# Performance work log

Measured on AMD Instinct MI355X. Metric: run time of the kernel, lower is better.

Reference implementation:

```python
import jax, jax.numpy as jnp
import numpy as np

N, E = 50000, 150000
IN, HID, LAT, EF, HE = 16, 32, 16, 8, 128


def _p(k, shape, fan_in):
    return jax.random.normal(k, shape, jnp.float32) / np.float32(np.sqrt(fan_in))


def setup_inputs() -> dict:
    key = jax.random.key(0)
    ks = jax.random.split(key, 32)
    inp = {
        "x": jax.random.normal(ks[0], (N, IN), jnp.float32),
        "edge_index": jax.random.randint(ks[1], (2, E), 0, N, dtype=jnp.int64),
        "edge_attr": jax.random.uniform(ks[2], (E, EF), jnp.float32),
    }
    # per-conv params: edge-MLP (w1,b1,w2,b2), root weight, bias
    dims = {"c1": (IN, HID), "c2": (HID, HID), "cmu": (HID, LAT), "clv": (HID, LAT)}
    i = 3
    for name, (din, dout) in dims.items():
        inp[f"{name}_w1"] = _p(ks[i], (EF, HE), EF)
        inp[f"{name}_b1"] = jnp.zeros((HE,), jnp.float32)
        inp[f"{name}_w2"] = _p(ks[i + 1], (HE, din * dout), HE)
        inp[f"{name}_b2"] = jnp.zeros((din * dout,), jnp.float32)
        inp[f"{name}_root"] = _p(ks[i + 2], (din, dout), din)
        inp[f"{name}_bias"] = jnp.zeros((dout,), jnp.float32)
        i += 3
    return inp


def _nnconv(x, src, dst, ea, w1, b1, w2, b2, root, bias, din, dout, mean):
    # edge MLP -> per-edge weight matrix [E, din, dout]
    h = jax.nn.relu(ea @ w1 + b1)
    W = (h @ w2 + b2).reshape(-1, din, dout)
    # gather source features, per-edge matmul, scatter-reduce to targets
    msg = jnp.einsum('ei,eio->eo', x[src], W)  # [E, dout]
    agg = jax.ops.segment_sum(msg, dst, num_segments=x.shape[0])
    if mean:
        cnt = jax.ops.segment_sum(jnp.ones((dst.shape[0],), x.dtype), dst,
                                  num_segments=x.shape[0])
        agg = agg / jnp.maximum(cnt, 1.0)[:, None]
    return agg + x @ root + bias


def reference(x, edge_index, edge_attr,
              c1_w1, c1_b1, c1_w2, c1_b2, c1_root, c1_bias,
              c2_w1, c2_b1, c2_w2, c2_b2, c2_root, c2_bias,
              cmu_w1, cmu_b1, cmu_w2, cmu_b2, cmu_root, cmu_bias,
              clv_w1, clv_b1, clv_w2, clv_b2, clv_root, clv_bias):
    src, dst = edge_index[0], edge_index[1]
    h = jax.nn.relu(_nnconv(x, src, dst, edge_attr, c1_w1, c1_b1, c1_w2, c1_b2,
                            c1_root, c1_bias, IN, HID, True))
    h = jax.nn.relu(_nnconv(h, src, dst, edge_attr, c2_w1, c2_b1, c2_w2, c2_b2,
                            c2_root, c2_bias, HID, HID, True))
    mu = _nnconv(h, src, dst, edge_attr, cmu_w1, cmu_b1, cmu_w2, cmu_b2,
                 cmu_root, cmu_bias, HID, LAT, False)
    logvar = _nnconv(h, src, dst, edge_attr, clv_w1, clv_b1, clv_w2, clv_b2,
                     clv_root, clv_bias, HID, LAT, False)
    return mu, logvar
```

## Files before the change

kernel.cpp:

```cpp
#include <hip/hip_runtime.h>

typedef __attribute__((ext_vector_type(8))) _Float16 half8;
typedef __attribute__((ext_vector_type(2))) _Float16 half2v;
typedef __attribute__((ext_vector_type(4))) float f32x4;

constexpr int NN  = 50000;
constexpr int NE  = 150000;
constexpr int IN  = 16;
constexpr int HID = 32;
constexpr int LAT = 16;
constexpr int EF  = 8;
constexpr int HE  = 128;
constexpr int NTILE = NE / 16;
constexpr int HSTR  = HE + 2;

constexpr int SCB = 256;
constexpr int NSB = (NN + SCB - 1) / SCB;

__global__ void count_kernel(const int* __restrict__ dst, int* __restrict__ cnt) {
  int e = blockIdx.x * blockDim.x + threadIdx.x;
  if (e < NE) atomicAdd(&cnt[dst[e]], 1);
}

__launch_bounds__(SCB)
__global__ void scan1(const int* __restrict__ cnt, int* __restrict__ bsum) {
  __shared__ int sdata[SCB];
  const int i = blockIdx.x * SCB + threadIdx.x;
  sdata[threadIdx.x] = (i < NN) ? cnt[i] : 0;
  __syncthreads();
  for (int off = SCB / 2; off > 0; off >>= 1) {
    if (threadIdx.x < off) sdata[threadIdx.x] += sdata[threadIdx.x + off];
    __syncthreads();
  }
  if (threadIdx.x == 0) bsum[blockIdx.x] = sdata[0];
}

__launch_bounds__(SCB)
__global__ void scan2(int* __restrict__ bsum) {
  __shared__ int sdata[SCB];
  const int t = threadIdx.x;
  const int v = (t < NSB) ? bsum[t] : 0;
  sdata[t] = v;
  __syncthreads();
  for (int off = 1; off < SCB; off <<= 1) {
    int u = (t >= off) ? sdata[t - off] : 0;
    __syncthreads();
    sdata[t] += u;
    __syncthreads();
  }
  if (t < NSB) bsum[t] = sdata[t] - v;
}

__launch_bounds__(SCB)
__global__ void scan3(const int* __restrict__ cnt, const int* __restrict__ bsum,
                      int* __restrict__ rowptr, int* __restrict__ wptr) {
  __shared__ int sdata[SCB];
  const int i = blockIdx.x * SCB + threadIdx.x;
  const int t = threadIdx.x;
  const int v = (i < NN) ? cnt[i] : 0;
  sdata[t] = v;
  __syncthreads();
  for (int off = 1; off < SCB; off <<= 1) {
    int u = (t >= off) ? sdata[t - off] : 0;
    __syncthreads();
    sdata[t] += u;
    __syncthreads();
  }
  const int excl = sdata[t] - v + bsum[blockIdx.x];
  if (i < NN) {
    rowptr[i] = excl;
    wptr[i]   = excl;
  }
  if (i == NN - 1) rowptr[NN] = NE;
}

__global__ void fill_kernel(const int* __restrict__ dst, int* __restrict__ wptr,
                            int* __restrict__ epos) {
  int e = blockIdx.x * blockDim.x + threadIdx.x;
  if (e < NE) epos[e] = atomicAdd(&wptr[dst[e]], 1);
}

__global__ void swizzle_kernel(const float* __restrict__ w2, const float* __restrict__ b2,
                               _Float16* __restrict__ w2h, int DIN_, int DOUT_) {
  int idx = blockIdx.x * blockDim.x + threadIdx.x;
  int tot = HSTR * DIN_ * DOUT_;
  if (idx >= tot) return;
  int i  = idx % DIN_;
  int o  = (idx / DIN_) % DOUT_;
  int kk = idx / (DIN_ * DOUT_);
  float v = 0.0f;
  if (kk < HE)       v = w2[(size_t)kk * DIN_ * DOUT_ + i * DOUT_ + o];
  else if (kk == HE) v = b2[i * DOUT_ + o];
  w2h[idx] = (_Float16)v;
}

template <int DIN, int DOUT>
__launch_bounds__(128)
__global__ void nnconv_mfma(const float* __restrict__ xin,
                            const int*   __restrict__ src,
                            const float* __restrict__ ea,
                            const float* __restrict__ w1,
                            const float* __restrict__ b1,
                            const _Float16* __restrict__ w2h,
                            const int*   __restrict__ epos,
                            float* __restrict__ msg)
{
  constexpr int OT     = DOUT / 16;
  constexpr int STEPS  = (DIN == 32) ? (HE + 1) : (HE + 2) / 2;
  constexpr int KKSTEP = 32 / DIN;
  constexpr int BSTRIDE = KKSTEP * DOUT * DIN;

  __shared__ float    ea_s[64 * EF];
  __shared__ _Float16 h_s[64 * HSTR];

  const int tid = threadIdx.x;
  const int eb  = blockIdx.x * 64;

  {
    int e = eb + (tid >> 1);
    float4 v = make_float4(0.f, 0.f, 0.f, 0.f);
    if (e < NE) v = *((const float4*)(ea + (size_t)e * EF) + (tid & 1));
    ((float4*)ea_s)[tid] = v;
  }
  __syncthreads();

  {
    const int kk = tid;
    float w1r[EF];
#pragma unroll
    for (int i = 0; i < EF; i++) w1r[i] = w1[i * HE + kk];
    const float bk = b1[kk];
#pragma unroll 4
    for (int e = 0; e < 64; e++) {
      float hv = bk;
#pragma unroll
      for (int i = 0; i < EF; i++) hv = fmaf(ea_s[e * EF + i], w1r[i], hv);
      hv = fmaxf(hv, 0.0f);
      h_s[e * HSTR + kk] = (_Float16)hv;
    }
    if (tid < 64) {
      h_s[tid * HSTR + HE]     = (_Float16)1.0f;
      h_s[tid * HSTR + HE + 1] = (_Float16)0.0f;
    }
  }
  __syncthreads();

  const int wave = tid >> 6;
  const int lane = tid & 63;
  const int m = lane & 15, q = lane >> 4;
  const int tg0 = blockIdx.x * 4 + wave * 2;

  const int i0 = (q * 8) % DIN;
  const int kq = (q * 8) / DIN;

  half2v xv[2][4];
#pragma unroll
  for (int t2 = 0; t2 < 2; t2++) {
    const int tg = tg0 + t2;
    if (tg < NTILE) {
      const int s = src[tg * 16 + m];
      const float4* xp = (const float4*)(xin + (size_t)s * DIN + i0);
      float4 a = xp[0], b = xp[1];
      xv[t2][0] = (half2v){(_Float16)a.x, (_Float16)a.y};
      xv[t2][1] = (half2v){(_Float16)a.z, (_Float16)a.w};
      xv[t2][2] = (half2v){(_Float16)b.x, (_Float16)b.y};
      xv[t2][3] = (half2v){(_Float16)b.z, (_Float16)b.w};
    } else {
#pragma unroll
      for (int j = 0; j < 4; j++) xv[t2][j] = (half2v){(_Float16)0.f, (_Float16)0.f};
    }
  }

  f32x4 acc[2][OT];
#pragma unroll
  for (int t2 = 0; t2 < 2; t2++)
#pragma unroll
    for (int ot = 0; ot < OT; ot++) acc[t2][ot] = (f32x4){0.f, 0.f, 0.f, 0.f};

  const _Float16* bp[OT];
#pragma unroll
  for (int ot = 0; ot < OT; ot++)
    bp[ot] = w2h + (size_t)(kq * DOUT + ot * 16 + m) * DIN + i0;

  const int hrow0 = wave * 32 + 0 * 16 + m;
  const int hrow1 = wave * 32 + 1 * 16 + m;

#pragma unroll 2
  for (int t = 0; t < STEPS; t++) {
    half8 bfr[OT];
#pragma unroll
    for (int ot = 0; ot < OT; ot++)
      bfr[ot] = *(const half8*)(bp[ot] + (size_t)t * BSTRIDE);

    const int kkidx = t * KKSTEP + kq;
#pragma unroll
    for (int t2 = 0; t2 < 2; t2++) {
      const int hrow = (t2 == 0) ? hrow0 : hrow1;
      const _Float16 hv = h_s[hrow * HSTR + kkidx];
      const half2v hb = (half2v){hv, hv};
      union { half2v h2[4]; half8 h8; } af;
#pragma unroll
      for (int j = 0; j < 4; j++) af.h2[j] = xv[t2][j] * hb;
#pragma unroll
      for (int ot = 0; ot < OT; ot++)
        acc[t2][ot] = __builtin_amdgcn_mfma_f32_16x16x32_f16(
            af.h8, bfr[ot], acc[t2][ot], 0, 0, 0);
    }
  }

#pragma unroll
  for (int t2 = 0; t2 < 2; t2++) {
    const int tg = tg0 + t2;
    if (tg < NTILE) {
      const int ebase = tg * 16 + q * 4;
      const int4 ep = *(const int4*)(epos + ebase);
      const int pr[4] = {ep.x, ep.y, ep.z, ep.w};
#pragma unroll
      for (int ot = 0; ot < OT; ot++)
#pragma unroll
        for (int r = 0; r < 4; r++)
          msg[(size_t)pr[r] * DOUT + ot * 16 + m] = acc[t2][ot][r];
    }
  }
}

template <int DIN, int DOUT, bool MEAN, bool RELU>
__launch_bounds__(256)
__global__ void finish_kernel(const float* __restrict__ msg,
                              const int* __restrict__ rowptr,
                              const float* __restrict__ xin,
                              const float* __restrict__ root,
                              const float* __restrict__ bias,
                              float* __restrict__ out) {
  constexpr int TPN = DOUT / 4;
  const int gid = blockIdx.x * 256 + threadIdx.x;
  const int n = gid / TPN, sub = gid % TPN;
  if (n >= NN) return;
  const int o0 = sub * 4;

  const int r0 = rowptr[n], r1 = rowptr[n + 1];
  float ax = 0.f, ay = 0.f, az = 0.f, aw = 0.f;
  for (int idx = r0; idx < r1; idx++) {
    const float4 mv = *(const float4*)(msg + (size_t)idx * DOUT + o0);
    ax += mv.x; ay += mv.y; az += mv.z; aw += mv.w;
  }
  const float inv = MEAN ? 1.0f / fmaxf((float)(r1 - r0), 1.0f) : 1.0f;
  float vx = ax * inv + bias[o0 + 0];
  float vy = ay * inv + bias[o0 + 1];
  float vz = az * inv + bias[o0 + 2];
  float vw = aw * inv + bias[o0 + 3];
#pragma unroll
  for (int i = 0; i < DIN; i++) {
    const float xi = xin[(size_t)n * DIN + i];
    const float4 rv = *(const float4*)(root + (size_t)i * DOUT + o0);
    vx = fmaf(xi, rv.x, vx); vy = fmaf(xi, rv.y, vy);
    vz = fmaf(xi, rv.z, vz); vw = fmaf(xi, rv.w, vw);
  }
  if (RELU) {
    vx = fmaxf(vx, 0.f); vy = fmaxf(vy, 0.f);
    vz = fmaxf(vz, 0.f); vw = fmaxf(vw, 0.f);
  }
  float4 o = make_float4(vx, vy, vz, vw);
  *(float4*)(out + (size_t)n * DOUT + o0) = o;
}

extern "C" void kernel_launch(void* const* d_in, const int* in_sizes, int n_in,
                              void* d_out, int out_size, void* d_ws, size_t ws_size,
                              hipStream_t stream) {
  const float* x  = (const float*)d_in[0];
  const int*   ei = (const int*)d_in[1];
  const float* ea = (const float*)d_in[2];
  const int* src = ei;
  const int* dst = ei + NE;

  auto P = [&](int c, int j) -> const float* {
    return (const float*)d_in[3 + c * 6 + j];
  };

  float* h1  = (float*)d_ws;
  float* h2  = h1 + (size_t)NN * HID;
  float* msg = h2 + (size_t)NN * HID;
  int* cnt    = (int*)(msg + (size_t)NE * 32);
  int* rowptr = cnt + NN;
  int* wptr   = rowptr + 50004;
  int* epos   = wptr + 50004;
  int* bsum   = epos + NE;
  _Float16* w2h_c1 = (_Float16*)(bsum + 256);
  _Float16* w2h_c2 = w2h_c1 + (size_t)HSTR * 32 * 16;
  _Float16* w2h_mu = w2h_c2 + (size_t)HSTR * 32 * 32;
  _Float16* w2h_lv = w2h_mu + (size_t)HSTR * 16 * 32;

  float* out_mu = (float*)d_out;
  float* out_lv = out_mu + (size_t)NN * LAT;

  hipMemsetAsync(cnt, 0, (size_t)NN * sizeof(int), stream);
  count_kernel<<<dim3((NE + 255) / 256), dim3(256), 0, stream>>>(dst, cnt);
  scan1<<<dim3(NSB), dim3(SCB), 0, stream>>>(cnt, bsum);
  scan2<<<dim3(1), dim3(SCB), 0, stream>>>(bsum);
  scan3<<<dim3(NSB), dim3(SCB), 0, stream>>>(cnt, bsum, rowptr, wptr);
  fill_kernel<<<dim3((NE + 255) / 256), dim3(256), 0, stream>>>(dst, wptr, epos);

  {
    int t1 = HSTR * 16 * 32, t2 = HSTR * 32 * 32, t3 = HSTR * 32 * 16;
    swizzle_kernel<<<dim3((t1 + 255) / 256), dim3(256), 0, stream>>>(
        P(0, 2), P(0, 3), w2h_c1, IN, HID);
    swizzle_kernel<<<dim3((t2 + 255) / 256), dim3(256), 0, stream>>>(
        P(1, 2), P(1, 3), w2h_c2, HID, HID);
    swizzle_kernel<<<dim3((t3 + 255) / 256), dim3(256), 0, stream>>>(
        P(2, 2), P(2, 3), w2h_mu, HID, LAT);
    swizzle_kernel<<<dim3((t3 + 255) / 256), dim3(256), 0, stream>>>(
        P(3, 2), P(3, 3), w2h_lv, HID, LAT);
  }

  const dim3 egrid((NTILE + 3) / 4), eblk(128);

  nnconv_mfma<IN, HID><<<egrid, eblk, 0, stream>>>(
      x, src, ea, P(0, 0), P(0, 1), w2h_c1, epos, msg);
  finish_kernel<IN, HID, true, true>
      <<<dim3((NN * (HID / 4) + 255) / 256), dim3(256), 0, stream>>>(
          msg, rowptr, x, P(0, 4), P(0, 5), h1);

  nnconv_mfma<HID, HID><<<egrid, eblk, 0, stream>>>(
      h1, src, ea, P(1, 0), P(1, 1), w2h_c2, epos, msg);
  finish_kernel<HID, HID, true, true>
      <<<dim3((NN * (HID / 4) + 255) / 256), dim3(256), 0, stream>>>(
          msg, rowptr, h1, P(1, 4), P(1, 5), h2);

  nnconv_mfma<HID, LAT><<<egrid, eblk, 0, stream>>>(
      h2, src, ea, P(2, 0), P(2, 1), w2h_mu, epos, msg);
  finish_kernel<HID, LAT, false, false>
      <<<dim3((NN * (LAT / 4) + 255) / 256), dim3(256), 0, stream>>>(
          msg, rowptr, h2, P(2, 4), P(2, 5), out_mu);

  nnconv_mfma<HID, LAT><<<egrid, eblk, 0, stream>>>(
      h2, src, ea, P(3, 0), P(3, 1), w2h_lv, epos, msg);
  finish_kernel<HID, LAT, false, false>
      <<<dim3((NN * (LAT / 4) + 255) / 256), dim3(256), 0, stream>>>(
          msg, rowptr, h2, P(3, 4), P(3, 5), out_lv);
}
```

Measured before the change: 423.9 us.

## Fuse mu/logvar convs into one dual kernel and store messages in fp16

The mu and logvar NNConv layers share the same input h2, so they are merged into a single edge kernel that gathers x once, builds the edge-MLP hidden layer for each head in turn, and writes two message arrays. A matching finish_dual kernel reduces both heads in one pass. The intermediate message buffer is also switched from fp32 to fp16, halving the scatter-write and gather-read traffic. This lowers precision of the aggregated sums, and the loop unroll changes from 2 to 4.

```diff
diff --git a/kernel.cpp b/kernel.cpp
--- a/kernel.cpp
+++ b/kernel.cpp
@@ -1,6 +1,7 @@
 #include <hip/hip_runtime.h>
 
 typedef __attribute__((ext_vector_type(8))) _Float16 half8;
+typedef __attribute__((ext_vector_type(4))) _Float16 half4v;
 typedef __attribute__((ext_vector_type(2))) _Float16 half2v;
 typedef __attribute__((ext_vector_type(4))) float f32x4;
 
@@ -94,20 +95,23 @@
   w2h[idx] = (_Float16)v;
 }
 
-template <int DIN, int DOUT>
+template <int DIN, int DOUT, bool DUAL>
 __launch_bounds__(128)
 __global__ void nnconv_mfma(const float* __restrict__ xin,
                             const int*   __restrict__ src,
                             const float* __restrict__ ea,
-                            const float* __restrict__ w1,
-                            const float* __restrict__ b1,
-                            const _Float16* __restrict__ w2h,
+                            const float* __restrict__ w1A,
+                            const float* __restrict__ b1A,
+                            const float* __restrict__ w1B,
+                            const float* __restrict__ b1B,
+                            const _Float16* __restrict__ w2hA,
+                            const _Float16* __restrict__ w2hB,
                             const int*   __restrict__ epos,
-                            float* __restrict__ msg)
+                            _Float16* __restrict__ msgA,
+                            _Float16* __restrict__ msgB)
 {
-  constexpr int OT     = DOUT / 16;
-  constexpr int STEPS  = (DIN == 32) ? (HE + 1) : (HE + 2) / 2;
-  constexpr int KKSTEP = 32 / DIN;
+  constexpr int STEPS   = (DIN == 32) ? (HE + 1) : (HE + 2) / 2;
+  constexpr int KKSTEP  = 32 / DIN;
   constexpr int BSTRIDE = KKSTEP * DOUT * DIN;
 
   __shared__ float    ea_s[64 * EF];
@@ -124,7 +128,7 @@
   }
   __syncthreads();
 
-  {
+  auto build_h = [&](const float* __restrict__ w1, const float* __restrict__ b1) {
     const int kk = tid;
     float w1r[EF];
 #pragma unroll
@@ -142,7 +146,9 @@
       h_s[tid * HSTR + HE]     = (_Float16)1.0f;
       h_s[tid * HSTR + HE + 1] = (_Float16)0.0f;
     }
-  }
+  };
+
+  build_h(w1A, b1A);
   __syncthreads();
 
   const int wave = tid >> 6;
@@ -171,40 +177,78 @@
     }
   }
 
-  f32x4 acc[2][OT];
+  f32x4 acc[2][2];
 #pragma unroll
   for (int t2 = 0; t2 < 2; t2++)
 #pragma unroll
-    for (int ot = 0; ot < OT; ot++) acc[t2][ot] = (f32x4){0.f, 0.f, 0.f, 0.f};
-
-  const _Float16* bp[OT];
-#pragma unroll
-  for (int ot = 0; ot < OT; ot++)
-    bp[ot] = w2h + (size_t)(kq * DOUT + ot * 16 + m) * DIN + i0;
-
-  const int hrow0 = wave * 32 + 0 * 16 + m;
-  const int hrow1 = wave * 32 + 1 * 16 + m;
-
-#pragma unroll 2
-  for (int t = 0; t < STEPS; t++) {
-    half8 bfr[OT];
-#pragma unroll
-    for (int ot = 0; ot < OT; ot++)
-      bfr[ot] = *(const half8*)(bp[ot] + (size_t)t * BSTRIDE);
-
-    const int kkidx = t * KKSTEP + kq;
-#pragma unroll
-    for (int t2 = 0; t2 < 2; t2++) {
-      const int hrow = (t2 == 0) ? hrow0 : hrow1;
-      const _Float16 hv = h_s[hrow * HSTR + kkidx];
-      const half2v hb = (half2v){hv, hv};
-      union { half2v h2[4]; half8 h8; } af;
-#pragma unroll
-      for (int j = 0; j < 4; j++) af.h2[j] = xv[t2][j] * hb;
-#pragma unroll
-      for (int ot = 0; ot < OT; ot++)
-        acc[t2][ot] = __builtin_amdgcn_mfma_f32_16x16x32_f16(
-            af.h8, bfr[ot], acc[t2][ot], 0, 0, 0);
+    for (int f = 0; f < 2; f++) acc[t2][f] = (f32x4){0.f, 0.f, 0.f, 0.f};
+
+  const int hrow0 = wave * 32 + m;
+  const int hrow1 = wave * 32 + 16 + m;
+
+  if constexpr (DUAL) {
+    {
+      const _Float16* bp = w2hA + (size_t)(kq * DOUT + m) * DIN + i0;
+#pragma unroll 4
+      for (int t = 0; t < STEPS; t++) {
+        const half8 bfr = *(const half8*)(bp + (size_t)t * BSTRIDE);
+        const int kkidx = t * KKSTEP + kq;
+#pragma unroll
+        for (int t2 = 0; t2 < 2; t2++) {
+          const int hrow = (t2 == 0) ? hrow0 : hrow1;
+          const _Float16 hv = h_s[hrow * HSTR + kkidx];
+          const half2v hb = (half2v){hv, hv};
+          union { half2v h2[4]; half8 h8; } af;
+#pragma unroll
+          for (int j = 0; j < 4; j++) af.h2[j] = xv[t2][j] * hb;
+          acc[t2][0] = __builtin_amdgcn_mfma_f32_16x16x32_f16(af.h8, bfr,
+                                                              acc[t2][0], 0, 0, 0);
+        }
+      }
+    }
+    __syncthreads();
+    build_h(w1B, b1B);
+    __syncthreads();
+    {
+      const _Float16* bp = w2hB + (size_t)(kq * DOUT + m) * DIN + i0;
+#pragma unroll 4
+      for (int t = 0; t < STEPS; t++) {
+        const half8 bfr = *(const half8*)(bp + (size_t)t * BSTRIDE);
+        const int kkidx = t * KKSTEP + kq;
+#pragma unroll
+        for (int t2 = 0; t2 < 2; t2++) {
+          const int hrow = (t2 == 0) ? hrow0 : hrow1;
+          const _Float16 hv = h_s[hrow * HSTR + kkidx];
+          const half2v hb = (half2v){hv, hv};
+          union { half2v h2[4]; half8 h8; } af;
+#pragma unroll
+          for (int j = 0; j < 4; j++) af.h2[j] = xv[t2][j] * hb;
+          acc[t2][1] = __builtin_amdgcn_mfma_f32_16x16x32_f16(af.h8, bfr,
+                                                              acc[t2][1], 0, 0, 0);
+        }
+      }
+    }
+  } else {
+    const _Float16* bp0 = w2hA + (size_t)(kq * DOUT + 0 + m) * DIN + i0;
+    const _Float16* bp1 = w2hA + (size_t)(kq * DOUT + 16 + m) * DIN + i0;
+#pragma unroll 4
+    for (int t = 0; t < STEPS; t++) {
+      const half8 bfr0 = *(const half8*)(bp0 + (size_t)t * BSTRIDE);
+      const half8 bfr1 = *(const half8*)(bp1 + (size_t)t * BSTRIDE);
+      const int kkidx = t * KKSTEP + kq;
+#pragma unroll
+      for (int t2 = 0; t2 < 2; t2++) {
+        const int hrow = (t2 == 0) ? hrow0 : hrow1;
+        const _Float16 hv = h_s[hrow * HSTR + kkidx];
+        const half2v hb = (half2v){hv, hv};
+        union { half2v h2[4]; half8 h8; } af;
+#pragma unroll
+        for (int j = 0; j < 4; j++) af.h2[j] = xv[t2][j] * hb;
+        acc[t2][0] = __builtin_amdgcn_mfma_f32_16x16x32_f16(af.h8, bfr0,
+                                                            acc[t2][0], 0, 0, 0);
+        acc[t2][1] = __builtin_amdgcn_mfma_f32_16x16x32_f16(af.h8, bfr1,
+                                                            acc[t2][1], 0, 0, 0);
+      }
     }
   }
 
@@ -215,18 +259,26 @@
       const int ebase = tg * 16 + q * 4;
       const int4 ep = *(const int4*)(epos + ebase);
       const int pr[4] = {ep.x, ep.y, ep.z, ep.w};
-#pragma unroll
-      for (int ot = 0; ot < OT; ot++)
-#pragma unroll
-        for (int r = 0; r < 4; r++)
-          msg[(size_t)pr[r] * DOUT + ot * 16 + m] = acc[t2][ot][r];
+      if (DUAL) {
+#pragma unroll
+        for (int r = 0; r < 4; r++) {
+          msgA[(size_t)pr[r] * DOUT + m] = (_Float16)acc[t2][0][r];
+          msgB[(size_t)pr[r] * DOUT + m] = (_Float16)acc[t2][1][r];
+        }
+      } else {
+#pragma unroll
+        for (int f = 0; f < 2; f++)
+#pragma unroll
+          for (int r = 0; r < 4; r++)
+            msgA[(size_t)pr[r] * DOUT + f * 16 + m] = (_Float16)acc[t2][f][r];
+      }
     }
   }
 }
 
 template <int DIN, int DOUT, bool MEAN, bool RELU>
 __launch_bounds__(256)
-__global__ void finish_kernel(const float* __restrict__ msg,
+__global__ void finish_kernel(const _Float16* __restrict__ msg,
                               const int* __restrict__ rowptr,
                               const float* __restrict__ xin,
                               const float* __restrict__ root,
@@ -241,8 +293,8 @@
   const int r0 = rowptr[n], r1 = rowptr[n + 1];
   float ax = 0.f, ay = 0.f, az = 0.f, aw = 0.f;
   for (int idx = r0; idx < r1; idx++) {
-    const float4 mv = *(const float4*)(msg + (size_t)idx * DOUT + o0);
-    ax += mv.x; ay += mv.y; az += mv.z; aw += mv.w;
+    const half4v mv = *(const half4v*)(msg + (size_t)idx * DOUT + o0);
+    ax += (float)mv.x; ay += (float)mv.y; az += (float)mv.z; aw += (float)mv.w;
   }
   const float inv = MEAN ? 1.0f / fmaxf((float)(r1 - r0), 1.0f) : 1.0f;
   float vx = ax * inv + bias[o0 + 0];
@@ -260,8 +312,52 @@
     vx = fmaxf(vx, 0.f); vy = fmaxf(vy, 0.f);
     vz = fmaxf(vz, 0.f); vw = fmaxf(vw, 0.f);
   }
-  float4 o = make_float4(vx, vy, vz, vw);
-  *(float4*)(out + (size_t)n * DOUT + o0) = o;
+  *(float4*)(out + (size_t)n * DOUT + o0) = make_float4(vx, vy, vz, vw);
+}
+
+template <int DIN>
+__launch_bounds__(256)
+__global__ void finish_dual(const _Float16* __restrict__ msgA,
+                            const _Float16* __restrict__ msgB,
+                            const int* __restrict__ rowptr,
+                            const float* __restrict__ xin,
+                            const float* __restrict__ rootA,
+                            const float* __restrict__ biasA,
+                            const float* __restrict__ rootB,
+                            const float* __restrict__ biasB,
+                            float* __restrict__ outA,
+                            float* __restrict__ outB) {
+  constexpr int TPN = LAT / 4;
+  const int gid = blockIdx.x * 256 + threadIdx.x;
+  const int n = gid / TPN, sub = gid % TPN;
+  if (n >= NN) return;
+  const int o0 = sub * 4;
+
+  const int r0 = rowptr[n], r1 = rowptr[n + 1];
+  float a0 = 0.f, a1 = 0.f, a2 = 0.f, a3 = 0.f;
+  float b0 = 0.f, b1 = 0.f, b2 = 0.f, b3 = 0.f;
+  for (int idx = r0; idx < r1; idx++) {
+    const half4v ma = *(const half4v*)(msgA + (size_t)idx * LAT + o0);
+    const half4v mb = *(const half4v*)(msgB + (size_t)idx * LAT + o0);
+    a0 += (float)ma.x; a1 += (float)ma.y; a2 += (float)ma.z; a3 += (float)ma.w;
+    b0 += (float)mb.x; b1 += (float)mb.y; b2 += (float)mb.z; b3 += (float)mb.w;
+  }
+  float va0 = a0 + biasA[o0 + 0], va1 = a1 + biasA[o0 + 1];
+  float va2 = a2 + biasA[o0 + 2], va3 = a3 + biasA[o0 + 3];
+  float vb0 = b0 + biasB[o0 + 0], vb1 = b1 + biasB[o0 + 1];
+  float vb2 = b2 + biasB[o0 + 2], vb3 = b3 + biasB[o0 + 3];
+#pragma unroll
+  for (int i = 0; i < DIN; i++) {
+    const float xi = xin[(size_t)n * DIN + i];
+    const float4 ra = *(const float4*)(rootA + (size_t)i * LAT + o0);
+    const float4 rb = *(const float4*)(rootB + (size_t)i * LAT + o0);
+    va0 = fmaf(xi, ra.x, va0); va1 = fmaf(xi, ra.y, va1);
+    va2 = fmaf(xi, ra.z, va2); va3 = fmaf(xi, ra.w, va3);
+    vb0 = fmaf(xi, rb.x, vb0); vb1 = fmaf(xi, rb.y, vb1);
+    vb2 = fmaf(xi, rb.z, vb2); vb3 = fmaf(xi, rb.w, vb3);
+  }
+  *(float4*)(outA + (size_t)n * LAT + o0) = make_float4(va0, va1, va2, va3);
+  *(float4*)(outB + (size_t)n * LAT + o0) = make_float4(vb0, vb1, vb2, vb3);
 }
 
 extern "C" void kernel_launch(void* const* d_in, const int* in_sizes, int n_in,
@@ -279,7 +375,7 @@
 
   float* h1  = (float*)d_ws;
   float* h2  = h1 + (size_t)NN * HID;
-  float* msg = h2 + (size_t)NN * HID;
+  _Float16* msg = (_Float16*)(h2 + (size_t)NN * HID);
   int* cnt    = (int*)(msg + (size_t)NE * 32);
   int* rowptr = cnt + NN;
   int* wptr   = rowptr + 50004;
@@ -289,6 +385,9 @@
   _Float16* w2h_c2 = w2h_c1 + (size_t)HSTR * 32 * 16;
   _Float16* w2h_mu = w2h_c2 + (size_t)HSTR * 32 * 32;
   _Float16* w2h_lv = w2h_mu + (size_t)HSTR * 16 * 32;
+
+  _Float16* msgA = msg;
+  _Float16* msgB = msg + (size_t)NE * 16;
 
   float* out_mu = (float*)d_out;
   float* out_lv = out_mu + (size_t)NN * LAT;
@@ -314,27 +413,25 @@
 
   const dim3 egrid((NTILE + 3) / 4), eblk(128);
 
-  nnconv_mfma<IN, HID><<<egrid, eblk, 0, stream>>>(
-      x, src, ea, P(0, 0), P(0, 1), w2h_c1, epos, msg);
+  nnconv_mfma<IN, HID, false><<<egrid, eblk, 0, stream>>>(
+      x, src, ea, P(0, 0), P(0, 1), nullptr, nullptr, w2h_c1, nullptr,
+      epos, msg, nullptr);
   finish_kernel<IN, HID, true, true>
       <<<dim3((NN * (HID / 4) + 255) / 256), dim3(256), 0, stream>>>(
           msg, rowptr, x, P(0, 4), P(0, 5), h1);
 
-  nnconv_mfma<HID, HID><<<egrid, eblk, 0, stream>>>(
-      h1, src, ea, P(1, 0), P(1, 1), w2h_c2, epos, msg);
+  nnconv_mfma<HID, HID, false><<<egrid, eblk, 0, stream>>>(
+      h1, src, ea, P(1, 0), P(1, 1), nullptr, nullptr, w2h_c2, nullptr,
+      epos, msg, nullptr);
   finish_kernel<HID, HID, true, true>
       <<<dim3((NN * (HID / 4) + 255) / 256), dim3(256), 0, stream>>>(
           msg, rowptr, h1, P(1, 4), P(1, 5), h2);
 
-  nnconv_mfma<HID, LAT><<<egrid, eblk, 0, stream>>>(
-      h2, src, ea, P(2, 0), P(2, 1), w2h_mu, epos, msg);
-  finish_kernel<HID, LAT, false, false>
+  nnconv_mfma<HID, LAT, true><<<egrid, eblk, 0, stream>>>(
+      h2, src, ea, P(2, 0), P(2, 1), P(3, 0), P(3, 1), w2h_mu, w2h_lv,
+      epos, msgA, msgB);
+  finish_dual<HID>
       <<<dim3((NN * (LAT / 4) + 255) / 256), dim3(256), 0, stream>>>(
-          msg, rowptr, h2, P(2, 4), P(2, 5), out_mu);
-
-  nnconv_mfma<HID, LAT><<<egrid, eblk, 0, stream>>>(
-      h2, src, ea, P(3, 0), P(3, 1), w2h_lv, epos, msg);
-  finish_kernel<HID, LAT, false, false>
-      <<<dim3((NN * (LAT / 4) + 255) / 256), dim3(256), 0, stream>>>(
-          msg, rowptr, h2, P(3, 4), P(3, 5), out_lv);
-}
+          msgA, msgB, rowptr, h2, P(2, 4), P(2, 5), P(3, 4), P(3, 5),
+          out_mu, out_lv);
+}
```

After: 401.1 us. -5.4%, faster.
